# Optimization experiments

Hardware: AMD Instinct MI355X
Metric: run time of the kernel (lower is better)

## Reference

```python
import jax, jax.numpy as jnp
import numpy as np

B, N, DIM = 1, 4096, 1024
HEADS, DIM_HEAD = 12, 8
POST_LOG_SCALE = 1.0
SCALE = DIM_HEAD ** -0.5


def setup_inputs() -> dict:
    key = jax.random.key(0)
    kx, kw = jax.random.split(key)
    x = jax.random.normal(kx, (B, N, DIM), dtype=jnp.float32)
    # torch nn.Linear(dim, heads*dim_head*2, bias=False) weight: [2*heads*dim_head, dim]
    W = jax.random.normal(kw, (2 * HEADS * DIM_HEAD, DIM), dtype=jnp.float32) * (DIM ** -0.5)
    return {"x": x, "W": W}


def reference(x, W):
    b, n, _ = x.shape
    # linear: x @ W^T -> [b, n, 2*h*d]; rearrange '(qk h d) -> qk b h n d'
    proj = jnp.einsum('bnc,oc->bno', x, W)
    proj = proj.reshape(b, n, 2, HEADS, DIM_HEAD)
    q = jnp.transpose(proj[:, :, 0], (0, 2, 1, 3))  # [b, h, n, d]
    k = jnp.transpose(proj[:, :, 1], (0, 2, 1, 3))  # [b, h, n, d]
    # small-d QK matmul -> [b, h, n, n]
    gates = jnp.einsum('bhid,bhjd->bhij', q, k) * SCALE
    gates = jax.nn.log_sigmoid(gates) * POST_LOG_SCALE
    # causal_mask = triu(ones, diagonal=0); masked_fill -> zero on/above diagonal
    i = jnp.arange(n)[:, None]
    j = jnp.arange(n)[None, :]
    keep = j < i  # strictly lower-triangular entries survive
    gates = jnp.where(keep, gates, 0.0)
    # flip-cumsum-flip == reverse cumulative sum along last axis
    gates = jax.lax.cumsum(gates, axis=3, reverse=True)
    return gates
```

## Files before the change

kernel.cpp:

```cpp
#include <hip/hip_runtime.h>

#define NTOK 4096
#define DIMC 1024
#define HEADS 12
#define DH 8
#define QSCALE 0.35355339059327373f
#define LOG2E  1.4426950408889634f
#define LN2    0.6931471805599453f
#define QPRE   (QSCALE * LOG2E)

typedef float f4 __attribute__((ext_vector_type(4)));
typedef float f2 __attribute__((ext_vector_type(2)));

#define KOFF (HEADS * NTOK * DH)

__global__ __launch_bounds__(256) void k1_proj(const float* __restrict__ x,
                                               const float* __restrict__ W,
                                               float* __restrict__ qk) {
    __shared__ float xs[8 * 1028];
    const int t = threadIdx.x;
    const int row0 = blockIdx.x * 8;

    const f4* x4 = (const f4*)(x + (size_t)row0 * DIMC);
    #pragma unroll
    for (int i = 0; i < 8; ++i) {
        int f = t + i * 256;
        int r = f >> 8;
        int c4 = f & 255;
        f4 v = x4[f];
        *(f4*)(&xs[r * 1028 + c4 * 4]) = v;
    }
    __syncthreads();

    const int g  = t >> 2;
    const int rg = t & 3;

    f2 acc[2][3];
    #pragma unroll
    for (int a = 0; a < 2; ++a)
        #pragma unroll
        for (int m = 0; m < 3; ++m) acc[a][m] = (f2)(0.f);

    const float* w0 = W + (size_t)(3 * g) * DIMC;
    #pragma unroll 2
    for (int c = 0; c < DIMC; c += 4) {
        f4 w[3];
        #pragma unroll
        for (int m = 0; m < 3; ++m)
            w[m] = *(const f4*)(w0 + (size_t)m * DIMC + c);
        #pragma unroll
        for (int a = 0; a < 2; ++a) {
            f4 xv = *(const f4*)(&xs[(rg * 2 + a) * 1028 + c]);
            #pragma unroll
            for (int m = 0; m < 3; ++m) {
                acc[a][m] = __builtin_elementwise_fma(xv.xy, w[m].xy, acc[a][m]);
                acc[a][m] = __builtin_elementwise_fma(xv.zw, w[m].zw, acc[a][m]);
            }
        }
    }

    #pragma unroll
    for (int m = 0; m < 3; ++m) {
        int o   = 3 * g + m;
        int qkf = (o >= 96) ? 1 : 0;
        int oo  = o - 96 * qkf;
        int h   = oo >> 3;
        int d   = oo & 7;
        #pragma unroll
        for (int a = 0; a < 2; ++a) {
            int n = row0 + rg * 2 + a;
            float v = acc[a][m].x + acc[a][m].y;
            if (!qkf) {
                qk[((size_t)h * NTOK + n) * DH + d] = v * QPRE;
            } else {
                qk[KOFF + (((size_t)h * 16 + (n >> 8)) * DH + d) * 256 + (n & 255)] = v;
            }
        }
    }
}

__device__ __forceinline__ float lsig2(float u) {
    float mn = fminf(u, 0.f);
    float z  = __builtin_amdgcn_exp2f(-fabsf(u));
    return mn - __builtin_amdgcn_logf(1.f + z);
}

__global__ __launch_bounds__(256) void k2_gates(const float* __restrict__ qk,
                                                float* __restrict__ out) {
    const int bid  = blockIdx.x;
    const int h    = bid >> 9;
    const int i0   = (bid & 511) << 3;
    const int t    = threadIdx.x;
    const int lane = t & 63;
    const int wid  = t >> 6;
    const int r0   = i0 + 2 * wid;
    const int r1   = r0 + 1;

    const float* qrow = qk + ((size_t)h * NTOK + r0) * DH;
    f2 q0s[8], q1s[8];
    #pragma unroll
    for (int d = 0; d < 8; ++d) {
        q0s[d] = (f2)(qrow[d]);
        q1s[d] = (f2)(qrow[DH + d]);
    }

    const float* kh = qk + KOFF + (size_t)h * (16 * DH * 256) + 4 * lane;
    float* o0 = out + ((size_t)h * NTOK + r0) * NTOK;
    float* o1 = o0 + NTOK;

    const int cb = r0 >> 8;

    f4 z = (f4)(0.f);
    for (int cc = 15; cc > cb; --cc) {
        const int j0 = cc * 256 + 4 * lane;
        *(f4*)(o0 + j0) = z;
        *(f4*)(o1 + j0) = z;
    }

    float carry0, carry1;

    f4 kv[8];
    {
        const float* kc = kh + (size_t)cb * (DH * 256);
        #pragma unroll
        for (int d = 0; d < 8; ++d) kv[d] = *(const f4*)(kc + d * 256);
    }

    {
        const int j0 = cb * 256 + 4 * lane;

        f2 A0 = (f2)(0.f), B0 = (f2)(0.f), A1 = (f2)(0.f), B1 = (f2)(0.f);
        #pragma unroll
        for (int d = 0; d < 8; ++d) {
            A0 = __builtin_elementwise_fma(kv[d].xy, q0s[d], A0);
            B0 = __builtin_elementwise_fma(kv[d].zw, q0s[d], B0);
            A1 = __builtin_elementwise_fma(kv[d].xy, q1s[d], A1);
            B1 = __builtin_elementwise_fma(kv[d].zw, q1s[d], B1);
        }

        {
            const int cn = (cb > 0) ? (cb - 1) : 0;
            const float* kn = kh + (size_t)cn * (DH * 256);
            #pragma unroll
            for (int d = 0; d < 8; ++d) kv[d] = *(const f4*)(kn + d * 256);
        }

        float g0[4], g1[4];
        g0[0] = (j0 + 0 < r0) ? lsig2(A0.x) : 0.f;
        g0[1] = (j0 + 1 < r0) ? lsig2(A0.y) : 0.f;
        g0[2] = (j0 + 2 < r0) ? lsig2(B0.x) : 0.f;
        g0[3] = (j0 + 3 < r0) ? lsig2(B0.y) : 0.f;
        g1[0] = (j0 + 0 < r1) ? lsig2(A1.x) : 0.f;
        g1[1] = (j0 + 1 < r1) ? lsig2(A1.y) : 0.f;
        g1[2] = (j0 + 2 < r1) ? lsig2(B1.x) : 0.f;
        g1[3] = (j0 + 3 < r1) ? lsig2(B1.y) : 0.f;

        g0[2] += g0[3]; g0[1] += g0[2]; g0[0] += g0[1];
        g1[2] += g1[3]; g1[1] += g1[2]; g1[0] += g1[1];
        const float t0 = g0[0], t1 = g1[0];
        float s0 = t0, s1 = t1;
        #pragma unroll
        for (int off = 1; off < 64; off <<= 1) {
            float v0 = __shfl_down(s0, off, 64);
            float v1 = __shfl_down(s1, off, 64);
            if (lane + off < 64) { s0 += v0; s1 += v1; }
        }
        const float base0 = s0 - t0;
        const float base1 = s1 - t1;
        carry0 = __builtin_amdgcn_readfirstlane(s0);
        carry1 = __builtin_amdgcn_readfirstlane(s1);

        f4 gv0 = {g0[0], g0[1], g0[2], g0[3]};
        f4 gv1 = {g1[0], g1[1], g1[2], g1[3]};
        *(f4*)(o0 + j0) = (gv0 + base0) * LN2;
        *(f4*)(o1 + j0) = (gv1 + base1) * LN2;
    }

    for (int cc = cb - 1; cc >= 0; --cc) {
        const int j0 = cc * 256 + 4 * lane;

        f2 A0 = (f2)(0.f), B0 = (f2)(0.f), A1 = (f2)(0.f), B1 = (f2)(0.f);
        #pragma unroll
        for (int d = 0; d < 8; ++d) {
            A0 = __builtin_elementwise_fma(kv[d].xy, q0s[d], A0);
            B0 = __builtin_elementwise_fma(kv[d].zw, q0s[d], B0);
            A1 = __builtin_elementwise_fma(kv[d].xy, q1s[d], A1);
            B1 = __builtin_elementwise_fma(kv[d].zw, q1s[d], B1);
        }

        {
            const int cn = (cc > 0) ? (cc - 1) : 0;
            const float* kn = kh + (size_t)cn * (DH * 256);
            #pragma unroll
            for (int d = 0; d < 8; ++d) kv[d] = *(const f4*)(kn + d * 256);
        }

        float g0[4], g1[4];
        g0[0] = lsig2(A0.x); g0[1] = lsig2(A0.y);
        g0[2] = lsig2(B0.x); g0[3] = lsig2(B0.y);
        g1[0] = lsig2(A1.x); g1[1] = lsig2(A1.y);
        g1[2] = lsig2(B1.x); g1[3] = lsig2(B1.y);

        g0[2] += g0[3]; g0[1] += g0[2]; g0[0] += g0[1];
        g1[2] += g1[3]; g1[1] += g1[2]; g1[0] += g1[1];
        const float t0 = g0[0], t1 = g1[0];
        float s0 = t0, s1 = t1;
        #pragma unroll
        for (int off = 1; off < 64; off <<= 1) {
            float v0 = __shfl_down(s0, off, 64);
            float v1 = __shfl_down(s1, off, 64);
            if (lane + off < 64) { s0 += v0; s1 += v1; }
        }
        const float base0 = (s0 - t0) + carry0;
        const float base1 = (s1 - t1) + carry1;
        carry0 += __builtin_amdgcn_readfirstlane(s0);
        carry1 += __builtin_amdgcn_readfirstlane(s1);

        f4 gv0 = {g0[0], g0[1], g0[2], g0[3]};
        f4 gv1 = {g1[0], g1[1], g1[2], g1[3]};
        *(f4*)(o0 + j0) = (gv0 + base0) * LN2;
        *(f4*)(o1 + j0) = (gv1 + base1) * LN2;
    }
}

extern "C" void kernel_launch(void* const* d_in, const int* in_sizes, int n_in,
                              void* d_out, int out_size, void* d_ws, size_t ws_size,
                              hipStream_t stream) {
    const float* x = (const float*)d_in[0];
    const float* W = (const float*)d_in[1];
    float* out = (float*)d_out;
    float* qk  = (float*)d_ws;

    hipLaunchKernelGGL(k1_proj, dim3(NTOK / 8), dim3(256), 0, stream, x, W, qk);
    hipLaunchKernelGGL(k2_gates, dim3(HEADS * NTOK / 8), dim3(256), 0, stream, qk, out);
}
```

Before: 210.5 us.

## Use persistent k2 blocks looping over rows with nontemporal stores and LDS occupancy cap

The gates kernel now launches 768 blocks, each covering 64 rows in 8 passes, instead of one block per 8 rows. All output stores become nontemporal so the 805MB write stream does not pollute the cache. A dummy 48KB shared array limits how many blocks fit per CU, which caps occupancy and likely eases write traffic contention. The risk is load imbalance, because each block's causal work grows with its row index and there are now fewer, larger blocks.

```diff
diff --git a/kernel.cpp b/kernel.cpp
--- a/kernel.cpp
+++ b/kernel.cpp
@@ -87,139 +87,143 @@
 
 __global__ __launch_bounds__(256) void k2_gates(const float* __restrict__ qk,
                                                 float* __restrict__ out) {
+    __shared__ float pad_[12288];
+    if (threadIdx.x == 0) ((volatile float*)pad_)[0] = 0.f;
+
     const int bid  = blockIdx.x;
-    const int h    = bid >> 9;
-    const int i0   = (bid & 511) << 3;
+    const int h    = bid >> 6;
+    const int s0   = (bid & 63) << 6;
     const int t    = threadIdx.x;
     const int lane = t & 63;
     const int wid  = t >> 6;
-    const int r0   = i0 + 2 * wid;
-    const int r1   = r0 + 1;
-
-    const float* qrow = qk + ((size_t)h * NTOK + r0) * DH;
-    f2 q0s[8], q1s[8];
-    #pragma unroll
-    for (int d = 0; d < 8; ++d) {
-        q0s[d] = (f2)(qrow[d]);
-        q1s[d] = (f2)(qrow[DH + d]);
-    }
 
     const float* kh = qk + KOFF + (size_t)h * (16 * DH * 256) + 4 * lane;
-    float* o0 = out + ((size_t)h * NTOK + r0) * NTOK;
-    float* o1 = o0 + NTOK;
-
-    const int cb = r0 >> 8;
-
-    f4 z = (f4)(0.f);
-    for (int cc = 15; cc > cb; --cc) {
-        const int j0 = cc * 256 + 4 * lane;
-        *(f4*)(o0 + j0) = z;
-        *(f4*)(o1 + j0) = z;
-    }
-
-    float carry0, carry1;
-
-    f4 kv[8];
-    {
-        const float* kc = kh + (size_t)cb * (DH * 256);
-        #pragma unroll
-        for (int d = 0; d < 8; ++d) kv[d] = *(const f4*)(kc + d * 256);
-    }
-
-    {
-        const int j0 = cb * 256 + 4 * lane;
-
-        f2 A0 = (f2)(0.f), B0 = (f2)(0.f), A1 = (f2)(0.f), B1 = (f2)(0.f);
+
+    for (int pass = 0; pass < 8; ++pass) {
+        const int r0 = s0 + pass * 8 + 2 * wid;
+        const int r1 = r0 + 1;
+
+        const float* qrow = qk + ((size_t)h * NTOK + r0) * DH;
+        f2 q0s[8], q1s[8];
         #pragma unroll
         for (int d = 0; d < 8; ++d) {
-            A0 = __builtin_elementwise_fma(kv[d].xy, q0s[d], A0);
-            B0 = __builtin_elementwise_fma(kv[d].zw, q0s[d], B0);
-            A1 = __builtin_elementwise_fma(kv[d].xy, q1s[d], A1);
-            B1 = __builtin_elementwise_fma(kv[d].zw, q1s[d], B1);
-        }
-
+            q0s[d] = (f2)(qrow[d]);
+            q1s[d] = (f2)(qrow[DH + d]);
+        }
+
+        float* o0 = out + ((size_t)h * NTOK + r0) * NTOK;
+        float* o1 = o0 + NTOK;
+        const int cb = r0 >> 8;
+
+        f4 z = (f4)(0.f);
+        for (int cc = 15; cc > cb; --cc) {
+            const int j0 = cc * 256 + 4 * lane;
+            __builtin_nontemporal_store(z, (f4*)(o0 + j0));
+            __builtin_nontemporal_store(z, (f4*)(o1 + j0));
+        }
+
+        float carry0, carry1;
+
+        f4 kv[8];
         {
-            const int cn = (cb > 0) ? (cb - 1) : 0;
-            const float* kn = kh + (size_t)cn * (DH * 256);
-            #pragma unroll
-            for (int d = 0; d < 8; ++d) kv[d] = *(const f4*)(kn + d * 256);
-        }
-
-        float g0[4], g1[4];
-        g0[0] = (j0 + 0 < r0) ? lsig2(A0.x) : 0.f;
-        g0[1] = (j0 + 1 < r0) ? lsig2(A0.y) : 0.f;
-        g0[2] = (j0 + 2 < r0) ? lsig2(B0.x) : 0.f;
-        g0[3] = (j0 + 3 < r0) ? lsig2(B0.y) : 0.f;
-        g1[0] = (j0 + 0 < r1) ? lsig2(A1.x) : 0.f;
-        g1[1] = (j0 + 1 < r1) ? lsig2(A1.y) : 0.f;
-        g1[2] = (j0 + 2 < r1) ? lsig2(B1.x) : 0.f;
-        g1[3] = (j0 + 3 < r1) ? lsig2(B1.y) : 0.f;
-
-        g0[2] += g0[3]; g0[1] += g0[2]; g0[0] += g0[1];
-        g1[2] += g1[3]; g1[1] += g1[2]; g1[0] += g1[1];
-        const float t0 = g0[0], t1 = g1[0];
-        float s0 = t0, s1 = t1;
-        #pragma unroll
-        for (int off = 1; off < 64; off <<= 1) {
-            float v0 = __shfl_down(s0, off, 64);
-            float v1 = __shfl_down(s1, off, 64);
-            if (lane + off < 64) { s0 += v0; s1 += v1; }
-        }
-        const float base0 = s0 - t0;
-        const float base1 = s1 - t1;
-        carry0 = __builtin_amdgcn_readfirstlane(s0);
-        carry1 = __builtin_amdgcn_readfirstlane(s1);
-
-        f4 gv0 = {g0[0], g0[1], g0[2], g0[3]};
-        f4 gv1 = {g1[0], g1[1], g1[2], g1[3]};
-        *(f4*)(o0 + j0) = (gv0 + base0) * LN2;
-        *(f4*)(o1 + j0) = (gv1 + base1) * LN2;
-    }
-
-    for (int cc = cb - 1; cc >= 0; --cc) {
-        const int j0 = cc * 256 + 4 * lane;
-
-        f2 A0 = (f2)(0.f), B0 = (f2)(0.f), A1 = (f2)(0.f), B1 = (f2)(0.f);
-        #pragma unroll
-        for (int d = 0; d < 8; ++d) {
-            A0 = __builtin_elementwise_fma(kv[d].xy, q0s[d], A0);
-            B0 = __builtin_elementwise_fma(kv[d].zw, q0s[d], B0);
-            A1 = __builtin_elementwise_fma(kv[d].xy, q1s[d], A1);
-            B1 = __builtin_elementwise_fma(kv[d].zw, q1s[d], B1);
+            const float* kc = kh + (size_t)cb * 2048;
+            #pragma unroll
+            for (int d = 0; d < 8; ++d) kv[d] = *(const f4*)(kc + d * 256);
         }
 
         {
-            const int cn = (cc > 0) ? (cc - 1) : 0;
-            const float* kn = kh + (size_t)cn * (DH * 256);
-            #pragma unroll
-            for (int d = 0; d < 8; ++d) kv[d] = *(const f4*)(kn + d * 256);
-        }
-
-        float g0[4], g1[4];
-        g0[0] = lsig2(A0.x); g0[1] = lsig2(A0.y);
-        g0[2] = lsig2(B0.x); g0[3] = lsig2(B0.y);
-        g1[0] = lsig2(A1.x); g1[1] = lsig2(A1.y);
-        g1[2] = lsig2(B1.x); g1[3] = lsig2(B1.y);
-
-        g0[2] += g0[3]; g0[1] += g0[2]; g0[0] += g0[1];
-        g1[2] += g1[3]; g1[1] += g1[2]; g1[0] += g1[1];
-        const float t0 = g0[0], t1 = g1[0];
-        float s0 = t0, s1 = t1;
-        #pragma unroll
-        for (int off = 1; off < 64; off <<= 1) {
-            float v0 = __shfl_down(s0, off, 64);
-            float v1 = __shfl_down(s1, off, 64);
-            if (lane + off < 64) { s0 += v0; s1 += v1; }
-        }
-        const float base0 = (s0 - t0) + carry0;
-        const float base1 = (s1 - t1) + carry1;
-        carry0 += __builtin_amdgcn_readfirstlane(s0);
-        carry1 += __builtin_amdgcn_readfirstlane(s1);
-
-        f4 gv0 = {g0[0], g0[1], g0[2], g0[3]};
-        f4 gv1 = {g1[0], g1[1], g1[2], g1[3]};
-        *(f4*)(o0 + j0) = (gv0 + base0) * LN2;
-        *(f4*)(o1 + j0) = (gv1 + base1) * LN2;
+            const int j0 = cb * 256 + 4 * lane;
+
+            f2 A0 = (f2)(0.f), B0 = (f2)(0.f), A1 = (f2)(0.f), B1 = (f2)(0.f);
+            #pragma unroll
+            for (int d = 0; d < 8; ++d) {
+                A0 = __builtin_elementwise_fma(kv[d].xy, q0s[d], A0);
+                B0 = __builtin_elementwise_fma(kv[d].zw, q0s[d], B0);
+                A1 = __builtin_elementwise_fma(kv[d].xy, q1s[d], A1);
+                B1 = __builtin_elementwise_fma(kv[d].zw, q1s[d], B1);
+            }
+            {
+                const int cn = (cb > 0) ? (cb - 1) : 0;
+                const float* kn = kh + (size_t)cn * 2048;
+                #pragma unroll
+                for (int d = 0; d < 8; ++d) kv[d] = *(const f4*)(kn + d * 256);
+            }
+
+            float g0[4], g1[4];
+            g0[0] = (j0 + 0 < r0) ? lsig2(A0.x) : 0.f;
+            g0[1] = (j0 + 1 < r0) ? lsig2(A0.y) : 0.f;
+            g0[2] = (j0 + 2 < r0) ? lsig2(B0.x) : 0.f;
+            g0[3] = (j0 + 3 < r0) ? lsig2(B0.y) : 0.f;
+            g1[0] = (j0 + 0 < r1) ? lsig2(A1.x) : 0.f;
+            g1[1] = (j0 + 1 < r1) ? lsig2(A1.y) : 0.f;
+            g1[2] = (j0 + 2 < r1) ? lsig2(B1.x) : 0.f;
+            g1[3] = (j0 + 3 < r1) ? lsig2(B1.y) : 0.f;
+
+            g0[2] += g0[3]; g0[1] += g0[2]; g0[0] += g0[1];
+            g1[2] += g1[3]; g1[1] += g1[2]; g1[0] += g1[1];
+            const float t0 = g0[0], t1 = g1[0];
+            float s0v = t0, s1v = t1;
+            #pragma unroll
+            for (int off = 1; off < 64; off <<= 1) {
+                float v0 = __shfl_down(s0v, off, 64);
+                float v1 = __shfl_down(s1v, off, 64);
+                if (lane + off < 64) { s0v += v0; s1v += v1; }
+            }
+            const float base0 = s0v - t0;
+            const float base1 = s1v - t1;
+            carry0 = __builtin_amdgcn_readfirstlane(s0v);
+            carry1 = __builtin_amdgcn_readfirstlane(s1v);
+
+            f4 gv0 = {g0[0], g0[1], g0[2], g0[3]};
+            f4 gv1 = {g1[0], g1[1], g1[2], g1[3]};
+            __builtin_nontemporal_store((gv0 + base0) * LN2, (f4*)(o0 + j0));
+            __builtin_nontemporal_store((gv1 + base1) * LN2, (f4*)(o1 + j0));
+        }
+
+        for (int cc = cb - 1; cc >= 0; --cc) {
+            const int j0 = cc * 256 + 4 * lane;
+
+            f2 A0 = (f2)(0.f), B0 = (f2)(0.f), A1 = (f2)(0.f), B1 = (f2)(0.f);
+            #pragma unroll
+            for (int d = 0; d < 8; ++d) {
+                A0 = __builtin_elementwise_fma(kv[d].xy, q0s[d], A0);
+                B0 = __builtin_elementwise_fma(kv[d].zw, q0s[d], B0);
+                A1 = __builtin_elementwise_fma(kv[d].xy, q1s[d], A1);
+                B1 = __builtin_elementwise_fma(kv[d].zw, q1s[d], B1);
+            }
+            {
+                const int cn = (cc > 0) ? (cc - 1) : 0;
+                const float* kn = kh + (size_t)cn * 2048;
+                #pragma unroll
+                for (int d = 0; d < 8; ++d) kv[d] = *(const f4*)(kn + d * 256);
+            }
+
+            float g0[4], g1[4];
+            g0[0] = lsig2(A0.x); g0[1] = lsig2(A0.y);
+            g0[2] = lsig2(B0.x); g0[3] = lsig2(B0.y);
+            g1[0] = lsig2(A1.x); g1[1] = lsig2(A1.y);
+            g1[2] = lsig2(B1.x); g1[3] = lsig2(B1.y);
+
+            g0[2] += g0[3]; g0[1] += g0[2]; g0[0] += g0[1];
+            g1[2] += g1[3]; g1[1] += g1[2]; g1[0] += g1[1];
+            const float t0 = g0[0], t1 = g1[0];
+            float s0v = t0, s1v = t1;
+            #pragma unroll
+            for (int off = 1; off < 64; off <<= 1) {
+                float v0 = __shfl_down(s0v, off, 64);
+                float v1 = __shfl_down(s1v, off, 64);
+                if (lane + off < 64) { s0v += v0; s1v += v1; }
+            }
+            const float base0 = (s0v - t0) + carry0;
+            const float base1 = (s1v - t1) + carry1;
+            carry0 += __builtin_amdgcn_readfirstlane(s0v);
+            carry1 += __builtin_amdgcn_readfirstlane(s1v);
+
+            f4 gv0 = {g0[0], g0[1], g0[2], g0[3]};
+            f4 gv1 = {g1[0], g1[1], g1[2], g1[3]};
+            __builtin_nontemporal_store((gv0 + base0) * LN2, (f4*)(o0 + j0));
+            __builtin_nontemporal_store((gv1 + base1) * LN2, (f4*)(o1 + j0));
+        }
     }
 }
 
@@ -232,5 +236,5 @@
     float* qk  = (float*)d_ws;
 
     hipLaunchKernelGGL(k1_proj, dim3(NTOK / 8), dim3(256), 0, stream, x, W, qk);
-    hipLaunchKernelGGL(k2_gates, dim3(HEADS * NTOK / 8), dim3(256), 0, stream, qk, out);
-}
+    hipLaunchKernelGGL(k2_gates, dim3(HEADS * 64), dim3(256), 0, stream, qk, out);
+}
```

Measured after the change: 250.9 us. +19.2%, slower.
